# Kernel optimization log

Measured on AMD Instinct MI355X. Metric: run time of the kernel, lower is better.

The kernel has to match this reference:

```python
import jax, jax.numpy as jnp
import numpy as np

EMBED_DIM = 1024
NUM_HEADS = 16
HEAD_DIM = EMBED_DIM // NUM_HEADS


def setup_inputs() -> dict:
    key = jax.random.key(0)
    ks = jax.random.split(key, 5)
    s = 1.0 / np.sqrt(EMBED_DIM)
    x = jax.random.normal(ks[0], (2, 2048, EMBED_DIM), dtype=jnp.float32)
    wq = jax.random.normal(ks[1], (EMBED_DIM, EMBED_DIM), dtype=jnp.float32) * s
    wk = jax.random.normal(ks[2], (EMBED_DIM, EMBED_DIM), dtype=jnp.float32) * s
    wv = jax.random.normal(ks[3], (EMBED_DIM, EMBED_DIM), dtype=jnp.float32) * s
    wo = jax.random.normal(ks[4], (EMBED_DIM, EMBED_DIM), dtype=jnp.float32) * s
    z = jnp.zeros((EMBED_DIM,), dtype=jnp.float32)
    return {"x": x, "wq": wq, "bq": z, "wk": wk, "bk": z, "wv": wv, "bv": z, "wo": wo, "bo": z}


def reference(x, wq, bq, wk, bk, wv, bv, wo, bo):
    B, S, D = x.shape
    H, Hd = NUM_HEADS, HEAD_DIM
    # projections -> [B, H, S, Hd]
    def proj(w, b):
        return (x @ w + b).reshape(B, S, H, Hd).transpose(0, 2, 1, 3)
    q = proj(wq, bq)
    k = proj(wk, bk)
    v = proj(wv, bv)
    scores = jnp.einsum('bhsd,bhtd->bhst', q, k) / jnp.sqrt(jnp.float32(Hd))
    probs = jax.nn.softmax(scores, axis=-1)
    attn = jnp.einsum('bhst,bhtd->bhsd', probs, v)  # [B,H,S,Hd]
    attn = attn.transpose(0, 2, 1, 3).reshape(B, S, D)
    return attn @ wo + bo
```

## Files before the change

### kernel.cpp

```cpp
#include <hip/hip_runtime.h>
#include <cstdint>

typedef __bf16 bf16_t;
typedef __bf16 bf16x4 __attribute__((ext_vector_type(4)));
typedef __bf16 bf16x8 __attribute__((ext_vector_type(8)));
typedef float floatx4 __attribute__((ext_vector_type(4)));

#define EMBED 1024
#define NHEAD 16
#define HDIM  64
#define SEQ   2048
#define BATCH 2
#define MTOT  (BATCH*SEQ)
#define QSCALE 0.18033688011112042f

__device__ __forceinline__ void gload16(const bf16_t* g, bf16_t* l) {
    __builtin_amdgcn_global_load_lds(
        (const __attribute__((address_space(1))) void*)g,
        (__attribute__((address_space(3))) void*)l, 16, 0, 0);
}

__device__ __forceinline__ void drain_dma() {
    asm volatile("s_waitcnt vmcnt(0)" ::: "memory");
}

__global__ __launch_bounds__(256) void transpose4(
    const float* __restrict__ w0, const float* __restrict__ w1,
    const float* __restrict__ w2, const float* __restrict__ w3,
    const float* __restrict__ xin,
    bf16_t* __restrict__ out, bf16_t* __restrict__ xout)
{
    int z = blockIdx.z;
    int tx = threadIdx.x, ty = threadIdx.y;
    if (z >= 4) {
        const float* src = xin  + (size_t)(z - 4) * 1048576u;
        bf16_t*      dst = xout + (size_t)(z - 4) * 1048576u;
        int col = blockIdx.x * 32 + tx, rowb = blockIdx.y * 32;
#pragma unroll
        for (int j = 0; j < 4; j++) {
            int rr = rowb + ty + 8 * j;
            dst[(size_t)rr * 1024 + col] = (bf16_t)src[(size_t)rr * 1024 + col];
        }
        return;
    }
    __shared__ float t[32][33];
    const float* src = (z == 0) ? w0 : (z == 1) ? w1 : (z == 2) ? w2 : w3;
    bf16_t* dst = out + (size_t)z * 1048576u;
    int bx = blockIdx.x * 32, by = blockIdx.y * 32;
#pragma unroll
    for (int j = 0; j < 4; j++)
        t[ty + 8 * j][tx] = src[(size_t)(by + ty + 8 * j) * EMBED + bx + tx];
    __syncthreads();
#pragma unroll
    for (int j = 0; j < 4; j++)
        dst[(size_t)(bx + ty + 8 * j) * EMBED + by + tx] = (bf16_t)t[tx][ty + 8 * j];
}

template<int BM, int MODE>
__global__ __launch_bounds__(256) void gemm_t(
    const bf16_t* __restrict__ A,  const bf16_t* __restrict__ Bt,
    const float* __restrict__ bias0, const float* __restrict__ bias1,
    const float* __restrict__ bias2,
    void* __restrict__ outraw, bf16_t* __restrict__ vtout,
    int M, int N, int K)
{
    constexpr int MS = BM / 32;
    constexpr int BUFSZ = (BM + 128) * 64;
    __shared__ __align__(16) bf16_t smem[2 * BUFSZ];

    int tid  = threadIdx.x;
    int id   = blockIdx.x;
    int c8   = id & 7, rr_ = id >> 3;
    int nblk = N >> 7;
    int n0   = (rr_ % nblk) * 128;
    int m0   = ((rr_ / nblk) * 8 + c8) * BM;
    int wv   = tid >> 6, lane = tid & 63;
    int wr   = wv >> 1,  wc   = wv & 1;
    int quad = lane >> 4, l16 = lane & 15;
    int lr   = lane >> 3, lq = lane & 7;
    int sw   = (l16 & 7) * 8;
    int lcs  = ((lq ^ lr) * 8);

    floatx4 acc[MS][4];
    floatx4 z4 = {0.f, 0.f, 0.f, 0.f};
#pragma unroll
    for (int mi = 0; mi < MS; mi++)
#pragma unroll
        for (int ni = 0; ni < 4; ni++) acc[mi][ni] = z4;

    auto STAGE = [&](int k0, int buf) {
        bf16_t* as = smem + buf * BUFSZ;
        bf16_t* bs = as + BM * 64;
#pragma unroll
        for (int i = 0; i < BM / 32; i++) {
            int r = wv * (BM / 4) + i * 8;
            gload16(&A[(size_t)(m0 + r + lr) * K + k0 + lcs], as + r * 64);
        }
#pragma unroll
        for (int i = 0; i < 4; i++) {
            int r = wv * 32 + i * 8;
            gload16(&Bt[(size_t)(n0 + r + lr) * K + k0 + lcs], bs + r * 64);
        }
    };

    STAGE(0, 0);
    int T = K >> 6;
    for (int t = 0; t < T; t++) {
        int cur = t & 1;
        drain_dma();
        __syncthreads();
        if (t + 1 < T) STAGE((t + 1) << 6, cur ^ 1);
        bf16_t (*As)[64] = (bf16_t(*)[64])(smem + cur * BUFSZ);
        bf16_t (*Bs)[64] = (bf16_t(*)[64])(smem + cur * BUFSZ + BM * 64);
#pragma unroll
        for (int kk = 0; kk < 2; kk++) {
            bf16x8 af[MS], bfr[4];
            int co = kk * 32 + quad * 8;
#pragma unroll
            for (int i = 0; i < MS; i++)
                af[i]  = *(const bf16x8*)&As[wr * (BM / 2) + i * 16 + l16][co ^ sw];
#pragma unroll
            for (int i = 0; i < 4; i++)
                bfr[i] = *(const bf16x8*)&Bs[wc * 64 + i * 16 + l16][co ^ sw];
#pragma unroll
            for (int mi = 0; mi < MS; mi++)
#pragma unroll
                for (int ni = 0; ni < 4; ni++)
                    acc[mi][ni] = __builtin_amdgcn_mfma_f32_16x16x32_bf16(
                        af[mi], bfr[ni], acc[mi][ni], 0, 0, 0);
        }
    }

    if constexpr (MODE == 1) {
        if (n0 >= 2048) {
            bf16_t (*Ts)[72] = (bf16_t(*)[72])smem;
            int bb = m0 >> 11, s0 = m0 & 2047;
            int hd0 = n0 & 1023;
#pragma unroll
            for (int mh = 0; mh < 2; mh++) {
                __syncthreads();
                if (wr == mh) {
#pragma unroll
                    for (int mi = 0; mi < MS; mi++)
#pragma unroll
                        for (int ni = 0; ni < 4; ni++)
#pragma unroll
                            for (int r = 0; r < 4; r++) {
                                int ml = mi * 16 + quad * 4 + r;
                                int nl = wc * 64 + ni * 16 + l16;
                                float v = acc[mi][ni][r] + bias2[hd0 + nl];
                                int sp = ((ml >> 5) << 5) | (((ml >> 2) & 3) << 3)
                                       | (((ml >> 4) & 1) << 2) | (ml & 3);
                                Ts[nl][sp] = (bf16_t)v;
                            }
                }
                __syncthreads();
#pragma unroll
                for (int i = 0; i < 4; i++) {
                    int c = tid + i * 256;
                    int row = c >> 3, ch = (c & 7) * 8;
                    int hh = row >> 6, dd = row & 63;
                    size_t off = (((size_t)bb * NHEAD + (hd0 >> 6) + hh) * HDIM + dd) * SEQ
                               + (size_t)(s0 + mh * 64 + ch);
                    *(bf16x8*)&vtout[off] = *(const bf16x8*)&Ts[row][ch];
                }
            }
            return;
        }
    }

#pragma unroll
    for (int mi = 0; mi < MS; mi++) {
#pragma unroll
        for (int ni = 0; ni < 4; ni++) {
            int n = n0 + wc * 64 + ni * 16 + l16;
#pragma unroll
            for (int r = 0; r < 4; r++) {
                int m = m0 + wr * (BM / 2) + mi * 16 + quad * 4 + r;
                float v = acc[mi][ni][r];
                if (MODE == 0) {
                    ((float*)outraw)[(size_t)m * N + n] = v + bias0[n];
                } else {
                    int which = n >> 10, cc = n & 1023;
                    v += (which == 0) ? bias0[cc] : bias1[cc];
                    if (which == 0) v *= QSCALE;
                    int h = cc >> 6, d = cc & 63;
                    int b = m >> 11, s = m & 2047;
                    ((bf16_t*)outraw)[(size_t)which * 4194304u +
                        (((size_t)b * NHEAD + h) * SEQ + s) * HDIM + d] = (bf16_t)v;
                }
            }
        }
    }
}

__global__ __launch_bounds__(256) void attn_mfma(
    const bf16_t* __restrict__ Q, const bf16_t* __restrict__ K,
    const bf16_t* __restrict__ Vt, bf16_t* __restrict__ O)
{
    __shared__ __align__(16) bf16_t Ks[2][64][64];
    __shared__ __align__(16) bf16_t Vs[2][64][64];

    int tid  = threadIdx.x;
    int wv   = tid >> 6, lane = tid & 63;
    int quad = lane >> 4, l16 = lane & 15;
    int lr   = lane >> 3, lq = lane & 7;
    int sw   = (l16 & 7) * 8;
    int flat = blockIdx.x;
    int hb   = flat & 31;
    int qt   = flat >> 5;
    int h = hb & 15, b = hb >> 4;
    int bh = b * NHEAD + h;
    int qw = qt * 128 + wv * 32;

    const bf16_t* Qb = Q  + (size_t)bh * SEQ * HDIM;
    const bf16_t* Kb = K  + (size_t)bh * SEQ * HDIM;
    const bf16_t* Vb = Vt + (size_t)bh * SEQ * HDIM;

    const bf16_t* kg = Kb + (size_t)(wv * 16 + lr) * HDIM + (lq ^ lr) * 8;
    const bf16_t* vg = Vb + (size_t)(wv * 16 + lr) * SEQ  + (lq ^ lr) * 8;

    bf16x8 qf[2][2];
#pragma unroll
    for (int ms = 0; ms < 2; ms++)
#pragma unroll
        for (int kk = 0; kk < 2; kk++)
            qf[ms][kk] = *(const bf16x8*)
                &Qb[(size_t)(qw + ms * 16 + l16) * HDIM + kk * 32 + quad * 8];

    floatx4 o_acc[2][4];
    floatx4 z4  = {0.f, 0.f, 0.f, 0.f};
    floatx4 m16 = {-16.f, -16.f, -16.f, -16.f};
#pragma unroll
    for (int ms = 0; ms < 2; ms++)
#pragma unroll
        for (int nd = 0; nd < 4; nd++) o_acc[ms][nd] = z4;
    float l_i[2] = {0.f, 0.f};

    gload16(kg,           &Ks[0][wv * 16][0]);
    gload16(kg + 512,     &Ks[0][wv * 16 + 8][0]);
    gload16(vg,           &Vs[0][wv * 16][0]);
    gload16(vg + 8 * SEQ, &Vs[0][wv * 16 + 8][0]);

    for (int t = 0; t < 32; t++) {
        int cur = t & 1;
        asm volatile("s_waitcnt vmcnt(0)" ::: "memory");
        __syncthreads();
        if (t < 31) {
            const bf16_t* kn = kg + (size_t)(t + 1) * 4096;
            const bf16_t* vn = vg + (size_t)(t + 1) * 64;
            int nb = cur ^ 1;
            gload16(kn,           &Ks[nb][wv * 16][0]);
            gload16(kn + 512,     &Ks[nb][wv * 16 + 8][0]);
            gload16(vn,           &Vs[nb][wv * 16][0]);
            gload16(vn + 8 * SEQ, &Vs[nb][wv * 16 + 8][0]);
        }

        floatx4 st[2][4];
#pragma unroll
        for (int ms = 0; ms < 2; ms++)
#pragma unroll
            for (int ns = 0; ns < 4; ns++) st[ms][ns] = m16;
#pragma unroll
        for (int ns = 0; ns < 4; ns++) {
#pragma unroll
            for (int kk = 0; kk < 2; kk++) {
                bf16x8 kf = *(const bf16x8*)
                    &Ks[cur][ns * 16 + l16][(kk * 32 + quad * 8) ^ sw];
#pragma unroll
                for (int ms = 0; ms < 2; ms++)
                    st[ms][ns] = __builtin_amdgcn_mfma_f32_16x16x32_bf16(
                        kf, qf[ms][kk], st[ms][ns], 0, 0, 0);
            }
        }

        bf16x8 pf[2][2];
#pragma unroll
        for (int ms = 0; ms < 2; ms++) {
            float ls = 0.f;
#pragma unroll
            for (int kk = 0; kk < 2; kk++)
#pragma unroll
                for (int tt = 0; tt < 8; tt++) {
                    float p = __builtin_amdgcn_exp2f(st[ms][2 * kk + (tt >> 2)][tt & 3]);
                    ls += p;
                    pf[ms][kk][tt] = (bf16_t)p;
                }
            l_i[ms] += ls;
        }

#pragma unroll
        for (int nd = 0; nd < 4; nd++) {
#pragma unroll
            for (int kk = 0; kk < 2; kk++) {
                bf16x8 vf = *(const bf16x8*)
                    &Vs[cur][nd * 16 + l16][(kk * 32 + quad * 8) ^ sw];
#pragma unroll
                for (int ms = 0; ms < 2; ms++)
                    o_acc[ms][nd] = __builtin_amdgcn_mfma_f32_16x16x32_bf16(
                        vf, pf[ms][kk], o_acc[ms][nd], 0, 0, 0);
            }
        }
    }

#pragma unroll
    for (int ms = 0; ms < 2; ms++) {
        float l = l_i[ms];
        l += __shfl_xor(l, 16);
        l += __shfl_xor(l, 32);
        float inv = 1.f / l;
        int q = qw + ms * 16 + l16;
        bf16_t* ob = O + ((size_t)b * SEQ + q) * EMBED + h * HDIM;
#pragma unroll
        for (int nd = 0; nd < 4; nd++)
#pragma unroll
            for (int r = 0; r < 4; r++)
                ob[nd * 16 + quad * 4 + r] = (bf16_t)(o_acc[ms][nd][r] * inv);
    }
}

extern "C" void kernel_launch(void* const* d_in, const int* in_sizes, int n_in,
                              void* d_out, int out_size, void* d_ws, size_t ws_size,
                              hipStream_t stream)
{
    const float* x  = (const float*)d_in[0];
    const float* wq = (const float*)d_in[1];
    const float* bq = (const float*)d_in[2];
    const float* wk = (const float*)d_in[3];
    const float* bk = (const float*)d_in[4];
    const float* wv = (const float*)d_in[5];
    const float* bv = (const float*)d_in[6];
    const float* wo = (const float*)d_in[7];
    const float* bo = (const float*)d_in[8];

    char*   ws    = (char*)d_ws;
    bf16_t* Wt    = (bf16_t*)ws;
    bf16_t* Xb    = (bf16_t*)(ws + 8ull  * 1024 * 1024);
    bf16_t* QKV   = (bf16_t*)(ws + 16ull * 1024 * 1024);
    bf16_t* Vt    = (bf16_t*)(ws + 40ull * 1024 * 1024);
    bf16_t* attnO = (bf16_t*)(ws + 48ull * 1024 * 1024);
    float*  outp  = (float*)d_out;

    transpose4<<<dim3(32, 32, 8), dim3(32, 8), 0, stream>>>(
        wq, wk, wv, wo, x, Wt, Xb);

    gemm_t<128, 1><<<dim3(768), 256, 0, stream>>>(
        Xb, Wt, bq, bk, bv, QKV, Vt, MTOT, 3072, EMBED);

    attn_mfma<<<dim3(512), 256, 0, stream>>>(
        QKV, QKV + 4194304u, Vt, attnO);

    gemm_t<64, 0><<<dim3(512), 256, 0, stream>>>(
        attnO, Wt + 3u * 1048576u, bo, bo, bo, outp, nullptr, MTOT, EMBED, EMBED);
}
```

Before: 185.2 us.

## Split attention block across 8 waves with 16 query rows each and specialized staging

Each attention block now runs 512 threads (8 waves), each wave owning 16 query rows instead of 32, which halves per-wave registers and accumulators and doubles wave-level parallelism per block. K/V staging is split so four waves load K and four load V, and s_setprio brackets the MFMA phases to favor matrix issue over other waves. The cost is that each K/V tile in shared memory is reused by fewer rows per wave, there are more waves contending at each barrier, and the per-MFMA B-operand reuse across two query sub-tiles is lost.

```diff
diff --git a/kernel.cpp b/kernel.cpp
--- a/kernel.cpp
+++ b/kernel.cpp
@@ -194,7 +194,7 @@
     }
 }
 
-__global__ __launch_bounds__(256) void attn_mfma(
+__global__ __launch_bounds__(512) void attn_mfma(
     const bf16_t* __restrict__ Q, const bf16_t* __restrict__ K,
     const bf16_t* __restrict__ Vt, bf16_t* __restrict__ O)
 {
@@ -211,112 +211,101 @@
     int qt   = flat >> 5;
     int h = hb & 15, b = hb >> 4;
     int bh = b * NHEAD + h;
-    int qw = qt * 128 + wv * 32;
+    int qw = qt * 128 + wv * 16;
 
     const bf16_t* Qb = Q  + (size_t)bh * SEQ * HDIM;
     const bf16_t* Kb = K  + (size_t)bh * SEQ * HDIM;
     const bf16_t* Vb = Vt + (size_t)bh * SEQ * HDIM;
 
-    const bf16_t* kg = Kb + (size_t)(wv * 16 + lr) * HDIM + (lq ^ lr) * 8;
-    const bf16_t* vg = Vb + (size_t)(wv * 16 + lr) * SEQ  + (lq ^ lr) * 8;
-
-    bf16x8 qf[2][2];
-#pragma unroll
-    for (int ms = 0; ms < 2; ms++)
-#pragma unroll
-        for (int kk = 0; kk < 2; kk++)
-            qf[ms][kk] = *(const bf16x8*)
-                &Qb[(size_t)(qw + ms * 16 + l16) * HDIM + kk * 32 + quad * 8];
-
-    floatx4 o_acc[2][4];
+    int vwave = wv >> 2;
+    int wr16  = (wv & 3) * 16;
+    const bf16_t* sg = vwave
+        ? Vb + (size_t)(wr16 + lr) * SEQ  + (lq ^ lr) * 8
+        : Kb + (size_t)(wr16 + lr) * HDIM + (lq ^ lr) * 8;
+    const size_t tstep = vwave ? 64u : 4096u;
+    const size_t rstep = vwave ? 8u * SEQ : 8u * HDIM;
+
+    auto STAGE = [&](int t, int buf) {
+        const bf16_t* g = sg + (size_t)t * tstep;
+        bf16_t* l = vwave ? &Vs[buf][wr16][0] : &Ks[buf][wr16][0];
+        gload16(g, l);
+        gload16(g + rstep, l + 8 * 64);
+    };
+
+    bf16x8 qf[2];
+#pragma unroll
+    for (int kk = 0; kk < 2; kk++)
+        qf[kk] = *(const bf16x8*)
+            &Qb[(size_t)(qw + l16) * HDIM + kk * 32 + quad * 8];
+
+    floatx4 o_acc[4];
     floatx4 z4  = {0.f, 0.f, 0.f, 0.f};
     floatx4 m16 = {-16.f, -16.f, -16.f, -16.f};
 #pragma unroll
-    for (int ms = 0; ms < 2; ms++)
-#pragma unroll
-        for (int nd = 0; nd < 4; nd++) o_acc[ms][nd] = z4;
-    float l_i[2] = {0.f, 0.f};
-
-    gload16(kg,           &Ks[0][wv * 16][0]);
-    gload16(kg + 512,     &Ks[0][wv * 16 + 8][0]);
-    gload16(vg,           &Vs[0][wv * 16][0]);
-    gload16(vg + 8 * SEQ, &Vs[0][wv * 16 + 8][0]);
+    for (int nd = 0; nd < 4; nd++) o_acc[nd] = z4;
+    float l_i = 0.f;
+
+    STAGE(0, 0);
 
     for (int t = 0; t < 32; t++) {
         int cur = t & 1;
-        asm volatile("s_waitcnt vmcnt(0)" ::: "memory");
+        drain_dma();
         __syncthreads();
-        if (t < 31) {
-            const bf16_t* kn = kg + (size_t)(t + 1) * 4096;
-            const bf16_t* vn = vg + (size_t)(t + 1) * 64;
-            int nb = cur ^ 1;
-            gload16(kn,           &Ks[nb][wv * 16][0]);
-            gload16(kn + 512,     &Ks[nb][wv * 16 + 8][0]);
-            gload16(vn,           &Vs[nb][wv * 16][0]);
-            gload16(vn + 8 * SEQ, &Vs[nb][wv * 16 + 8][0]);
-        }
-
-        floatx4 st[2][4];
-#pragma unroll
-        for (int ms = 0; ms < 2; ms++)
-#pragma unroll
-            for (int ns = 0; ns < 4; ns++) st[ms][ns] = m16;
+        if (t < 31) STAGE(t + 1, cur ^ 1);
+
+        floatx4 st[4];
+#pragma unroll
+        for (int ns = 0; ns < 4; ns++) st[ns] = m16;
+        __builtin_amdgcn_s_setprio(1);
 #pragma unroll
         for (int ns = 0; ns < 4; ns++) {
 #pragma unroll
             for (int kk = 0; kk < 2; kk++) {
                 bf16x8 kf = *(const bf16x8*)
                     &Ks[cur][ns * 16 + l16][(kk * 32 + quad * 8) ^ sw];
-#pragma unroll
-                for (int ms = 0; ms < 2; ms++)
-                    st[ms][ns] = __builtin_amdgcn_mfma_f32_16x16x32_bf16(
-                        kf, qf[ms][kk], st[ms][ns], 0, 0, 0);
-            }
-        }
-
-        bf16x8 pf[2][2];
-#pragma unroll
-        for (int ms = 0; ms < 2; ms++) {
-            float ls = 0.f;
-#pragma unroll
-            for (int kk = 0; kk < 2; kk++)
-#pragma unroll
-                for (int tt = 0; tt < 8; tt++) {
-                    float p = __builtin_amdgcn_exp2f(st[ms][2 * kk + (tt >> 2)][tt & 3]);
-                    ls += p;
-                    pf[ms][kk][tt] = (bf16_t)p;
-                }
-            l_i[ms] += ls;
-        }
-
+                st[ns] = __builtin_amdgcn_mfma_f32_16x16x32_bf16(
+                    kf, qf[kk], st[ns], 0, 0, 0);
+            }
+        }
+        __builtin_amdgcn_s_setprio(0);
+
+        bf16x8 pf[2];
+        float ls = 0.f;
+#pragma unroll
+        for (int kk = 0; kk < 2; kk++)
+#pragma unroll
+            for (int tt = 0; tt < 8; tt++) {
+                float p = __builtin_amdgcn_exp2f(st[2 * kk + (tt >> 2)][tt & 3]);
+                ls += p;
+                pf[kk][tt] = (bf16_t)p;
+            }
+        l_i += ls;
+
+        __builtin_amdgcn_s_setprio(1);
 #pragma unroll
         for (int nd = 0; nd < 4; nd++) {
 #pragma unroll
             for (int kk = 0; kk < 2; kk++) {
                 bf16x8 vf = *(const bf16x8*)
                     &Vs[cur][nd * 16 + l16][(kk * 32 + quad * 8) ^ sw];
-#pragma unroll
-                for (int ms = 0; ms < 2; ms++)
-                    o_acc[ms][nd] = __builtin_amdgcn_mfma_f32_16x16x32_bf16(
-                        vf, pf[ms][kk], o_acc[ms][nd], 0, 0, 0);
-            }
-        }
-    }
-
-#pragma unroll
-    for (int ms = 0; ms < 2; ms++) {
-        float l = l_i[ms];
-        l += __shfl_xor(l, 16);
-        l += __shfl_xor(l, 32);
-        float inv = 1.f / l;
-        int q = qw + ms * 16 + l16;
-        bf16_t* ob = O + ((size_t)b * SEQ + q) * EMBED + h * HDIM;
-#pragma unroll
-        for (int nd = 0; nd < 4; nd++)
-#pragma unroll
-            for (int r = 0; r < 4; r++)
-                ob[nd * 16 + quad * 4 + r] = (bf16_t)(o_acc[ms][nd][r] * inv);
-    }
+                o_acc[nd] = __builtin_amdgcn_mfma_f32_16x16x32_bf16(
+                    vf, pf[kk], o_acc[nd], 0, 0, 0);
+            }
+        }
+        __builtin_amdgcn_s_setprio(0);
+    }
+
+    float l = l_i;
+    l += __shfl_xor(l, 16);
+    l += __shfl_xor(l, 32);
+    float inv = 1.f / l;
+    int q = qw + l16;
+    bf16_t* ob = O + ((size_t)b * SEQ + q) * EMBED + h * HDIM;
+#pragma unroll
+    for (int nd = 0; nd < 4; nd++)
+#pragma unroll
+        for (int r = 0; r < 4; r++)
+            ob[nd * 16 + quad * 4 + r] = (bf16_t)(o_acc[nd][r] * inv);
 }
 
 extern "C" void kernel_launch(void* const* d_in, const int* in_sizes, int n_in,
@@ -347,7 +336,7 @@
     gemm_t<128, 1><<<dim3(768), 256, 0, stream>>>(
         Xb, Wt, bq, bk, bv, QKV, Vt, MTOT, 3072, EMBED);
 
-    attn_mfma<<<dim3(512), 256, 0, stream>>>(
+    attn_mfma<<<dim3(512), 512, 0, stream>>>(
         QKV, QKV + 4194304u, Vt, attnO);
 
     gemm_t<64, 0><<<dim3(512), 256, 0, stream>>>(
```

Measured after the change: 179.7 us. 1.03x faster.
